# Kernel optimization log

Hardware: AMD Instinct MI355X
Metric: run time of the kernel (lower is better)

## Reference

```python
import jax, jax.numpy as jnp
import numpy as np

NUM_HEADS = 16
HEAD_DIM = 64  # model_dim // num_heads


def setup_inputs() -> dict:
    key = jax.random.key(0)
    ks = jax.random.split(key, 9)
    B, S, D = 2, 2048, 1024
    scale = 1.0 / np.sqrt(D)
    inp = {
        "tokens": jax.random.normal(ks[0], (B, S, D), dtype=jnp.float32),
        "Wq": jax.random.normal(ks[1], (D, D), dtype=jnp.float32) * scale,
        "bq": jnp.zeros((D,), dtype=jnp.float32),
        "Wk": jax.random.normal(ks[2], (D, D), dtype=jnp.float32) * scale,
        "bk": jnp.zeros((D,), dtype=jnp.float32),
        "Wv": jax.random.normal(ks[3], (D, D), dtype=jnp.float32) * scale,
        "bv": jnp.zeros((D,), dtype=jnp.float32),
        "Wo": jax.random.normal(ks[4], (D, D), dtype=jnp.float32) * scale,
        "bo": jnp.zeros((D,), dtype=jnp.float32),
    }
    return inp


def _split_heads(x):
    # [B, S, D] -> [B, H, S, d]
    B, S, D = x.shape
    return x.reshape(B, S, NUM_HEADS, HEAD_DIM).transpose(0, 2, 1, 3)


def reference(tokens, Wq, bq, Wk, bk, Wv, bv, Wo, bo):
    B, S, D = tokens.shape
    q = _split_heads(tokens @ Wq + bq)
    k = _split_heads(tokens @ Wk + bk)
    v = _split_heads(tokens @ Wv + bv)
    # shared logits: [B, H, S, S]
    logits = jnp.einsum("bhqd,bhkd->bhqk", q, k) / jnp.sqrt(
        jnp.asarray(HEAD_DIM, dtype=tokens.dtype))
    attn_neg = jax.nn.softmax(-logits, axis=-1)
    attn_pos = jax.nn.softmax(logits, axis=-1)
    feat_neg = jnp.einsum("bhqk,bhkd->bhqd", attn_neg, v)
    feat_pos = jnp.einsum("bhqk,bhkd->bhqd", attn_pos, v)
    # [B, H, S, d] -> [B, S, D]
    feat_neg = feat_neg.transpose(0, 2, 1, 3).reshape(B, S, D)
    feat_pos = feat_pos.transpose(0, 2, 1, 3).reshape(B, S, D)
    # shared output projection (proj[-1]) applied to both branches
    return (feat_neg @ Wo + bo, feat_pos @ Wo + bo)
```

## Files before the change

kernel.cpp:

```cpp
#include <hip/hip_runtime.h>
#include <hip/hip_bf16.h>

using bf16x8 = __attribute__((ext_vector_type(8))) short;
using f32x4  = __attribute__((ext_vector_type(4))) float;
using f32x16 = __attribute__((ext_vector_type(16))) float;
using u32x4  = __attribute__((ext_vector_type(4))) unsigned;

static constexpr int B_ = 2, S_ = 2048, D_ = 1024, H_ = 16, HD_ = 64;
static constexpr int BS_ = B_ * S_;
static constexpr float CP_ = 0.18033688011112042f;

__device__ __forceinline__ unsigned short bfbits(float x) {
    unsigned u = __builtin_bit_cast(unsigned, x);
    unsigned r = (u + 0x7fffu + ((u >> 16) & 1u)) >> 16;
    return (unsigned short)r;
}
__device__ __forceinline__ short bfs(float x) { return (short)bfbits(x); }

__device__ __forceinline__ unsigned cvt_pk_bf16(float lo, float hi) {
    unsigned r;
    asm("v_cvt_pk_bf16_f32 %0, %1, %2" : "=v"(r) : "v"(lo), "v"(hi));
    return r;
}
__device__ __forceinline__ void gload_lds16(const short* g, short* l) {
    __builtin_amdgcn_global_load_lds(
        (const __attribute__((address_space(1))) void*)g,
        (__attribute__((address_space(3))) void*)l, 16, 0, 0);
}

__global__ void cast_f32_bf16_kernel(const float* __restrict__ in,
                                     short* __restrict__ out, int n8) {
    int i = blockIdx.x * blockDim.x + threadIdx.x;
    if (i >= n8) return;
    const float4* p = (const float4*)in + (size_t)i * 2;
    float4 a = p[0], b = p[1];
    short tmp[8] = { bfs(a.x), bfs(a.y), bfs(a.z), bfs(a.w),
                     bfs(b.x), bfs(b.y), bfs(b.z), bfs(b.w) };
    *(int4*)(out + (size_t)i * 8) = *(int4*)tmp;
}

__global__ void transpose_cast4_kernel(const float* __restrict__ Wq,
                                       const float* __restrict__ Wk,
                                       const float* __restrict__ Wv,
                                       const float* __restrict__ Wo,
                                       short* __restrict__ WT) {
    __shared__ short tile[64][65];
    const float* srcs[4] = {Wq, Wk, Wv, Wo};
    const float* in = srcs[blockIdx.z];
    short* out = WT + (size_t)blockIdx.z * D_ * D_;
    int t = threadIdx.x;
    int r0 = blockIdx.y * 64, c0 = blockIdx.x * 64;
    int lr = t >> 2, lc0 = (t & 3) * 16;
    const float4* src = (const float4*)(in + (size_t)(r0 + lr) * D_ + c0 + lc0);
#pragma unroll
    for (int v = 0; v < 4; v++) {
        float4 f = src[v];
        tile[lr][lc0 + v * 4 + 0] = bfs(f.x);
        tile[lr][lc0 + v * 4 + 1] = bfs(f.y);
        tile[lr][lc0 + v * 4 + 2] = bfs(f.z);
        tile[lr][lc0 + v * 4 + 3] = bfs(f.w);
    }
    __syncthreads();
    int oc = t >> 2, os0 = (t & 3) * 16;
    short tmp[16];
#pragma unroll
    for (int j = 0; j < 16; j++) tmp[j] = tile[os0 + j][oc];
    short* dst = out + (size_t)(c0 + oc) * D_ + r0 + os0;
    *(int4*)(dst) = *(int4*)(tmp);
    *(int4*)(dst + 8) = *(int4*)(tmp + 8);
}

template <int MODE>
__global__ __launch_bounds__(256, 2)
void gemm_bt_kernel(const short* __restrict__ A, const short* __restrict__ BT,
                    const float* __restrict__ bp0, const float* __restrict__ bp1,
                    const float* __restrict__ bp2, void* __restrict__ Cout,
                    int M, int N, int K, int nBx, int cpx) {
    __shared__ __align__(16) short As[128 * 32];
    __shared__ __align__(16) short Bs[128 * 32];
    int bid = blockIdx.x;
    int wg = (bid & 7) * cpx + (bid >> 3);
    int bx = wg % nBx, by = wg / nBx;
    int t = threadIdx.x;
    int w = t >> 6, l = t & 63;
    int lq = l & 15, g = l >> 4;
    int rowBase = by * 128, colBase = bx * 128;
    int wrow = (w >> 1) * 64, wcol = (w & 1) * 64;
    f32x4 acc[4][4] = {};
    const short* ap0 = A + (size_t)(rowBase + (t >> 2)) * K + (t & 3) * 8;
    const short* ap1 = ap0 + (size_t)64 * K;
    const short* bpA = BT + (size_t)(colBase + (t >> 2)) * K + (t & 3) * 8;
    const short* bpB = bpA + (size_t)64 * K;
    for (int kt = 0; kt < K; kt += 32) {
        __syncthreads();
        gload_lds16(ap0 + kt, &As[t * 8]);
        gload_lds16(ap1 + kt, &As[t * 8 + 2048]);
        gload_lds16(bpA + kt, &Bs[t * 8]);
        gload_lds16(bpB + kt, &Bs[t * 8 + 2048]);
        __syncthreads();
        bf16x8 af[4], bfr[4];
#pragma unroll
        for (int mi = 0; mi < 4; mi++)
            af[mi] = *(const bf16x8*)(&As[(wrow + mi * 16 + lq) * 32 + 8 * g]);
#pragma unroll
        for (int ni = 0; ni < 4; ni++)
            bfr[ni] = *(const bf16x8*)(&Bs[(wcol + ni * 16 + lq) * 32 + 8 * g]);
#pragma unroll
        for (int mi = 0; mi < 4; mi++)
#pragma unroll
            for (int ni = 0; ni < 4; ni++)
                acc[mi][ni] = __builtin_amdgcn_mfma_f32_16x16x32_bf16(
                    af[mi], bfr[ni], acc[mi][ni], 0, 0, 0);
    }
#pragma unroll
    for (int mi = 0; mi < 4; mi++)
#pragma unroll
        for (int ni = 0; ni < 4; ni++) {
            int col = colBase + wcol + ni * 16 + lq;
            float bias, scale = 1.0f;
            if (MODE == 0) {
                const float* bp = (col < 1024) ? bp0 : ((col < 2048) ? bp1 : bp2);
                bias = bp[col & 1023];
                if (col < 1024) scale = CP_;
            } else {
                bias = bp0[col];
            }
#pragma unroll
            for (int r = 0; r < 4; r++) {
                int row = rowBase + wrow + mi * 16 + 4 * g + r;
                float v = (acc[mi][ni][r] + bias) * scale;
                if (MODE == 1)
                    ((float*)Cout)[(size_t)row * N + col] = v;
                else
                    ((short*)Cout)[(size_t)row * N + col] = bfs(v);
            }
        }
}

__global__ void pack_qk_kernel(const short* __restrict__ QKV,
                               short* __restrict__ Qf, short* __restrict__ Kf) {
    int t = threadIdx.x;
    int l = t & 63, hf = t >> 6;
    int tile = blockIdx.x;
    int h = blockIdx.y;
    int z = blockIdx.z; int b = z & 1, src = z >> 1;
    int s = tile * 32 + (l & 31);
    int d = 16 * hf + 8 * (l >> 5);
    const short* sp = QKV + (size_t)(b * S_ + s) * 3072 + src * 1024 + h * 64 + d;
    short* dst = (src ? Kf : Qf) +
                 ((((size_t)(b * H_ + h) * 64 + tile) * 4 + hf) * 64 + l) * 8;
    *(int4*)dst = *(const int4*)sp;
}

__global__ void pack_v_kernel(const short* __restrict__ QKV,
                              short* __restrict__ Vf) {
    __shared__ short Vl[256][68];
    int t = threadIdx.x;
    int sgrp = blockIdx.x, h = blockIdx.y, b = blockIdx.z;
    const short* sp = QKV + (size_t)(b * S_ + sgrp * 256 + t) * 3072 + 2048 + h * 64;
#pragma unroll
    for (int c = 0; c < 8; c++)
        *(int4*)(&Vl[t][c * 8]) = *(const int4*)(sp + c * 8);
    __syncthreads();
    int l = t & 63, hf = (t >> 6) & 1, dblk = t >> 7;
    int h2 = l >> 5, d = dblk * 32 + (l & 31);
    short* dstbase = Vf + (size_t)(b * H_ + h) * 131072;
#pragma unroll
    for (int k = 0; k < 8; k++) {
        short tmp[8];
#pragma unroll
        for (int j = 0; j < 8; j++) {
            int sl = k * 32 + 16 * hf + (j & 3) + 8 * (j >> 2) + 4 * h2;
            tmp[j] = Vl[sl][d];
        }
        int tile = sgrp * 8 + k;
        short* dst = dstbase + ((((size_t)tile * 2 + dblk) * 2 + hf) * 64 + l) * 8;
        *(int4*)dst = *(int4*)tmp;
    }
}

__global__ __launch_bounds__(256, 2)
void attn_kernel(const short* __restrict__ Qf, const short* __restrict__ Kf,
                 const short* __restrict__ Vf, short* __restrict__ featNeg,
                 short* __restrict__ featPos) {
    int bid = blockIdx.x;
    int wg = (bid & 7) * 64 + (bid >> 3);
    int qtile = wg & 15, hh = (wg >> 4) & 15, b = wg >> 8;
    int t = threadIdx.x;
    int w = t >> 6, l = t & 63;
    int l31 = l & 31, h2 = l >> 5;
    int qb0 = qtile * 128 + w * 32;
    size_t hb = (size_t)(b * H_ + hh) * 131072;

    bf16x8 qa[4];
    const short* qp = Qf + hb + ((size_t)(qb0 >> 5) * 4 * 64 + l) * 8;
#pragma unroll
    for (int hf = 0; hf < 4; hf++)
        qa[hf] = *(const bf16x8*)(qp + hf * 512);

    bf16x8 ones;
#pragma unroll
    for (int j = 0; j < 8; j++) ones[j] = (short)0x3F80;

    f32x16 acc[2][2] = {};
    f32x16 acc_l[2] = {};

    const short* kp0 = Kf + hb + l * 8;
    const short* vp0 = Vf + hb + l * 8;

#pragma unroll 2
    for (int tile = 0; tile < 64; tile++) {
        const short* kp = kp0 + (size_t)tile * 2048;
        const short* vp = vp0 + (size_t)tile * 2048;
        bf16x8 ka[4];
#pragma unroll
        for (int hf = 0; hf < 4; hf++)
            ka[hf] = *(const bf16x8*)(kp + hf * 512);
        bf16x8 vb[2][2];
#pragma unroll
        for (int dblk = 0; dblk < 2; dblk++)
#pragma unroll
            for (int hf = 0; hf < 2; hf++)
                vb[dblk][hf] = *(const bf16x8*)(vp + (dblk * 2 + hf) * 512);

        f32x16 st = {};
        __builtin_amdgcn_s_setprio(1);
#pragma unroll
        for (int hf = 0; hf < 4; hf++)
            st = __builtin_amdgcn_mfma_f32_32x32x16_bf16(ka[hf], qa[hf], st, 0, 0, 0);
        __builtin_amdgcn_s_setprio(0);

#pragma unroll
        for (int br = 0; br < 2; br++) {
            unsigned c[8];
#pragma unroll
            for (int i = 0; i < 8; i++) {
                float plo = __builtin_amdgcn_exp2f(br ? st[2 * i] : -st[2 * i]);
                float phi = __builtin_amdgcn_exp2f(br ? st[2 * i + 1] : -st[2 * i + 1]);
                c[i] = cvt_pk_bf16(plo, phi);
            }
            u32x4 lo4 = {c[0], c[1], c[2], c[3]};
            u32x4 hi4 = {c[4], c[5], c[6], c[7]};
            bf16x8 pa0 = __builtin_bit_cast(bf16x8, lo4);
            bf16x8 pa1 = __builtin_bit_cast(bf16x8, hi4);
            __builtin_amdgcn_s_setprio(1);
#pragma unroll
            for (int dblk = 0; dblk < 2; dblk++) {
                acc[br][dblk] = __builtin_amdgcn_mfma_f32_32x32x16_bf16(
                    pa0, vb[dblk][0], acc[br][dblk], 0, 0, 0);
                acc[br][dblk] = __builtin_amdgcn_mfma_f32_32x32x16_bf16(
                    pa1, vb[dblk][1], acc[br][dblk], 0, 0, 0);
            }
            acc_l[br] = __builtin_amdgcn_mfma_f32_32x32x16_bf16(pa0, ones, acc_l[br], 0, 0, 0);
            acc_l[br] = __builtin_amdgcn_mfma_f32_32x32x16_bf16(pa1, ones, acc_l[br], 0, 0, 0);
            __builtin_amdgcn_s_setprio(0);
        }
    }

#pragma unroll
    for (int br = 0; br < 2; br++) {
        short* dst = br ? featPos : featNeg;
#pragma unroll
        for (int r = 0; r < 16; r++) {
            int qr = (r & 3) + 8 * (r >> 2) + 4 * h2;
            float invq = 1.0f / acc_l[br][r];
            size_t row = (size_t)(b * S_ + qb0 + qr);
#pragma unroll
            for (int dblk = 0; dblk < 2; dblk++) {
                int col = hh * HD_ + dblk * 32 + l31;
                dst[row * D_ + col] = bfs(acc[br][dblk][r] * invq);
            }
        }
    }
}

extern "C" void kernel_launch(void* const* d_in, const int* in_sizes, int n_in,
                              void* d_out, int out_size, void* d_ws, size_t ws_size,
                              hipStream_t stream) {
    const float* tokens = (const float*)d_in[0];
    const float* Wq = (const float*)d_in[1];
    const float* bq = (const float*)d_in[2];
    const float* Wk = (const float*)d_in[3];
    const float* bk = (const float*)d_in[4];
    const float* Wv = (const float*)d_in[5];
    const float* bv = (const float*)d_in[6];
    const float* Wo = (const float*)d_in[7];
    const float* bo = (const float*)d_in[8];

    const size_t MB = 1048576;
    if (ws_size < 64 * MB) return;
    char* ws = (char*)d_ws;
    short* Xbf = (short*)(ws + 0 * MB);
    short* WT  = (short*)(ws + 8 * MB);
    short* QKV = (short*)(ws + 16 * MB);
    short* featNeg = (short*)(ws + 16 * MB);
    short* featPos = (short*)(ws + 24 * MB);
    short* Qf = (short*)(ws + 40 * MB);
    short* Kf = (short*)(ws + 48 * MB);
    short* Vf = (short*)(ws + 56 * MB);

    cast_f32_bf16_kernel<<<2048, 256, 0, stream>>>(tokens, Xbf, BS_ * D_ / 8);

    transpose_cast4_kernel<<<dim3(16, 16, 4), 256, 0, stream>>>(Wq, Wk, Wv, Wo, WT);

    gemm_bt_kernel<0><<<768, 256, 0, stream>>>(
        Xbf, WT, bq, bk, bv, QKV, BS_, 3072, D_, 24, 96);

    pack_qk_kernel<<<dim3(64, 16, 4), 256, 0, stream>>>(QKV, Qf, Kf);
    pack_v_kernel<<<dim3(8, 16, 2), 256, 0, stream>>>(QKV, Vf);

    attn_kernel<<<512, 256, 0, stream>>>(Qf, Kf, Vf, featNeg, featPos);

    gemm_bt_kernel<1><<<512, 256, 0, stream>>>(
        featNeg, WT + (size_t)3 * D_ * D_, bo, nullptr, nullptr, d_out,
        2 * BS_, D_, D_, 8, 64);
}
```

Measured before the change: 228.4 us.

## Double GEMM K-tile to 64 and compute softmax row sums on VALU

The projection GEMM now stages 64-wide K tiles in LDS and does two MFMA sub-steps per tile, halving the number of barrier-separated load phases at the cost of more LDS. In the attention kernel, the extra MFMAs that multiplied probabilities by a ones vector to get row sums are replaced by fp32 VALU accumulation plus a cross-half shuffle at the end. This removes a third of the PV-stage matrix instructions per branch but adds VALU adds and sums unrounded rather than bf16-rounded probabilities.

```diff
diff --git a/kernel.cpp b/kernel.cpp
--- a/kernel.cpp
+++ b/kernel.cpp
@@ -76,8 +76,8 @@
                     const float* __restrict__ bp0, const float* __restrict__ bp1,
                     const float* __restrict__ bp2, void* __restrict__ Cout,
                     int M, int N, int K, int nBx, int cpx) {
-    __shared__ __align__(16) short As[128 * 32];
-    __shared__ __align__(16) short Bs[128 * 32];
+    __shared__ __align__(16) short As[128 * 64];
+    __shared__ __align__(16) short Bs[128 * 64];
     int bid = blockIdx.x;
     int wg = (bid & 7) * cpx + (bid >> 3);
     int bx = wg % nBx, by = wg / nBx;
@@ -87,30 +87,32 @@
     int rowBase = by * 128, colBase = bx * 128;
     int wrow = (w >> 1) * 64, wcol = (w & 1) * 64;
     f32x4 acc[4][4] = {};
-    const short* ap0 = A + (size_t)(rowBase + (t >> 2)) * K + (t & 3) * 8;
-    const short* ap1 = ap0 + (size_t)64 * K;
-    const short* bpA = BT + (size_t)(colBase + (t >> 2)) * K + (t & 3) * 8;
-    const short* bpB = bpA + (size_t)64 * K;
-    for (int kt = 0; kt < K; kt += 32) {
+    const short* ap = A + (size_t)(rowBase + (t >> 3)) * K + (t & 7) * 8;
+    const short* bp = BT + (size_t)(colBase + (t >> 3)) * K + (t & 7) * 8;
+    for (int kt = 0; kt < K; kt += 64) {
         __syncthreads();
-        gload_lds16(ap0 + kt, &As[t * 8]);
-        gload_lds16(ap1 + kt, &As[t * 8 + 2048]);
-        gload_lds16(bpA + kt, &Bs[t * 8]);
-        gload_lds16(bpB + kt, &Bs[t * 8 + 2048]);
+#pragma unroll
+        for (int L = 0; L < 4; L++) {
+            gload_lds16(ap + (size_t)L * 32 * K + kt, &As[(L * 256 + t) * 8]);
+            gload_lds16(bp + (size_t)L * 32 * K + kt, &Bs[(L * 256 + t) * 8]);
+        }
         __syncthreads();
-        bf16x8 af[4], bfr[4];
-#pragma unroll
-        for (int mi = 0; mi < 4; mi++)
-            af[mi] = *(const bf16x8*)(&As[(wrow + mi * 16 + lq) * 32 + 8 * g]);
-#pragma unroll
-        for (int ni = 0; ni < 4; ni++)
-            bfr[ni] = *(const bf16x8*)(&Bs[(wcol + ni * 16 + lq) * 32 + 8 * g]);
-#pragma unroll
-        for (int mi = 0; mi < 4; mi++)
+#pragma unroll
+        for (int ks = 0; ks < 2; ks++) {
+            bf16x8 af[4], bfr[4];
+#pragma unroll
+            for (int mi = 0; mi < 4; mi++)
+                af[mi] = *(const bf16x8*)(&As[(wrow + mi * 16 + lq) * 64 + ks * 32 + 8 * g]);
 #pragma unroll
             for (int ni = 0; ni < 4; ni++)
-                acc[mi][ni] = __builtin_amdgcn_mfma_f32_16x16x32_bf16(
-                    af[mi], bfr[ni], acc[mi][ni], 0, 0, 0);
+                bfr[ni] = *(const bf16x8*)(&Bs[(wcol + ni * 16 + lq) * 64 + ks * 32 + 8 * g]);
+#pragma unroll
+            for (int mi = 0; mi < 4; mi++)
+#pragma unroll
+                for (int ni = 0; ni < 4; ni++)
+                    acc[mi][ni] = __builtin_amdgcn_mfma_f32_16x16x32_bf16(
+                        af[mi], bfr[ni], acc[mi][ni], 0, 0, 0);
+        }
     }
 #pragma unroll
     for (int mi = 0; mi < 4; mi++)
@@ -119,8 +121,8 @@
             int col = colBase + wcol + ni * 16 + lq;
             float bias, scale = 1.0f;
             if (MODE == 0) {
-                const float* bp = (col < 1024) ? bp0 : ((col < 2048) ? bp1 : bp2);
-                bias = bp[col & 1023];
+                const float* bpp = (col < 1024) ? bp0 : ((col < 2048) ? bp1 : bp2);
+                bias = bpp[col & 1023];
                 if (col < 1024) scale = CP_;
             } else {
                 bias = bp0[col];
@@ -198,12 +200,8 @@
     for (int hf = 0; hf < 4; hf++)
         qa[hf] = *(const bf16x8*)(qp + hf * 512);
 
-    bf16x8 ones;
-#pragma unroll
-    for (int j = 0; j < 8; j++) ones[j] = (short)0x3F80;
-
     f32x16 acc[2][2] = {};
-    f32x16 acc_l[2] = {};
+    float lsum[2] = {0.f, 0.f};
 
     const short* kp0 = Kf + hb + l * 8;
     const short* vp0 = Vf + hb + l * 8;
@@ -233,12 +231,15 @@
 #pragma unroll
         for (int br = 0; br < 2; br++) {
             unsigned c[8];
+            float s0 = 0.f, s1 = 0.f;
 #pragma unroll
             for (int i = 0; i < 8; i++) {
                 float plo = __builtin_amdgcn_exp2f(br ? st[2 * i] : -st[2 * i]);
                 float phi = __builtin_amdgcn_exp2f(br ? st[2 * i + 1] : -st[2 * i + 1]);
+                if (i & 1) s1 += plo + phi; else s0 += plo + phi;
                 c[i] = cvt_pk_bf16(plo, phi);
             }
+            lsum[br] += s0 + s1;
             u32x4 lo4 = {c[0], c[1], c[2], c[3]};
             u32x4 hi4 = {c[4], c[5], c[6], c[7]};
             bf16x8 pa0 = __builtin_bit_cast(bf16x8, lo4);
@@ -251,19 +252,20 @@
                 acc[br][dblk] = __builtin_amdgcn_mfma_f32_32x32x16_bf16(
                     pa1, vb[dblk][1], acc[br][dblk], 0, 0, 0);
             }
-            acc_l[br] = __builtin_amdgcn_mfma_f32_32x32x16_bf16(pa0, ones, acc_l[br], 0, 0, 0);
-            acc_l[br] = __builtin_amdgcn_mfma_f32_32x32x16_bf16(pa1, ones, acc_l[br], 0, 0, 0);
             __builtin_amdgcn_s_setprio(0);
         }
     }
 
 #pragma unroll
     for (int br = 0; br < 2; br++) {
+        float ls = lsum[br];
+        ls += __shfl_xor(ls, 32);
+        float inv = 1.0f / ls;
         short* dst = br ? featPos : featNeg;
 #pragma unroll
         for (int r = 0; r < 16; r++) {
             int qr = (r & 3) + 8 * (r >> 2) + 4 * h2;
-            float invq = 1.0f / acc_l[br][r];
+            float invq = __shfl(inv, qr);
             size_t row = (size_t)(b * S_ + qb0 + qr);
 #pragma unroll
             for (int dblk = 0; dblk < 2; dblk++) {
```

Measured after the change: 229.9 us. No clear change (+0.6%).
